# Kernel optimization log

Measured on AMD Instinct MI355X. Metric: run time of the kernel, lower is better.

Reference implementation:

```python
import jax, jax.numpy as jnp
import numpy as np

I_SIZE = 8      # interval_size
WS = 8          # window_size
SHIFT = 4       # window_size // 2
HG = 4          # grid-attn heads (num_heads // 2)
HS = 4          # swin/window heads (num_heads // 2)


def cln(x, g, b, eps=1e-5):
    # channel LayerNorm over axis 1 of NCHW
    mu = x.mean(axis=1, keepdims=True)
    var = ((x - mu) ** 2).mean(axis=1, keepdims=True)
    return (x - mu) / jnp.sqrt(var + eps) * g[None, :, None, None] + b[None, :, None, None]


def conv1x1(x, w, b):
    return jnp.einsum('bchw,oc->bohw', x, w) + b[None, :, None, None]


def grid_shuffle(x, I):
    B, C, H, W = x.shape
    H1, W1 = H // I, W // I
    x = x.reshape(B, C, H1, I, W1, I).transpose(0, 3, 5, 1, 2, 4)
    return x.reshape(B * I * I, C, H1, W1)


def grid_unshuffle(x, I):
    Bi, C, H1, W1 = x.shape
    B = Bi // (I * I)
    x = x.reshape(B, I, I, C, H1, W1).transpose(0, 3, 4, 1, 5, 2)
    return x.reshape(B, C, H1 * I, W1 * I)


def rel_pos_index(wh, ww):
    coords = np.stack(np.meshgrid(np.arange(wh), np.arange(ww), indexing='ij')).reshape(2, -1)
    rel = (coords[:, :, None] - coords[:, None, :]).transpose(1, 2, 0)
    rel[:, :, 0] += wh - 1
    rel[:, :, 1] += ww - 1
    rel[:, :, 0] *= 2 * ww - 1
    return rel.sum(-1)  # (N, N) int


def dyn_pos_bias(H1, W1, w1, b1, w2, b2, w3, b3):
    # dynamic position bias MLP: (2,) relative coords -> heads
    ch = np.arange(1 - H1, H1, dtype=np.float32)
    cw = np.arange(1 - W1, W1, dtype=np.float32)
    rel = np.stack(np.meshgrid(ch, cw, indexing='ij'), axis=-1).reshape(-1, 2)
    t = jnp.asarray(rel)
    t = jax.nn.relu(t @ w1.T + b1)
    t = jax.nn.relu(t @ w2.T + b2)
    t = t @ w3.T + b3  # ((2H1-1)*(2W1-1), heads)
    idx = rel_pos_index(H1, W1)
    return t[idx].transpose(2, 0, 1)[None]  # (1, heads, N, N)


def mha2d(q, k, v, bias, heads, pw, pb):
    B, C, H, W = q.shape
    hd, N = C // heads, H * W
    sp = lambda t: t.reshape(B, heads, hd, N).transpose(0, 1, 3, 2)
    qh, kh, vh = sp(q), sp(k), sp(v)
    attn = jax.nn.softmax(jnp.einsum('bhnd,bhmd->bhnm', qh * hd ** -0.5, kh) + bias, axis=-1)
    out = jnp.einsum('bhnm,bhmd->bhnd', attn, vh).transpose(0, 1, 3, 2).reshape(B, C, H, W)
    return conv1x1(out, pw, pb)


def swin_mask(H, W, ws, shift):
    img = np.zeros((H, W), np.float32)
    cnt = 0
    for hs in (slice(0, H - ws), slice(H - ws, H - shift), slice(H - shift, H)):
        for wsl in (slice(0, W - ws), slice(W - ws, W - shift), slice(W - shift, W)):
            img[hs, wsl] = cnt
            cnt += 1
    mw = img.reshape(H // ws, ws, W // ws, ws).transpose(0, 2, 1, 3).reshape(-1, ws * ws)
    m = mw[:, None, :] - mw[:, :, None]
    return jnp.asarray(np.where(m != 0, -100.0, 0.0).astype(np.float32))  # (nW, N, N)


def swin_attn(x, qkv_w, qkv_b, rpb, pw, pb, ws, shift, heads):
    B, C, H, W = x.shape
    hd, N = C // heads, ws * ws
    if shift > 0:
        x = jnp.roll(x, (-shift, -shift), axis=(2, 3))
    nh, nw = H // ws, W // ws
    nW = nh * nw
    xw = x.reshape(B, C, nh, ws, nw, ws).transpose(0, 2, 4, 3, 5, 1).reshape(B * nW, N, C)
    qkv = (xw @ qkv_w.T + qkv_b).reshape(B * nW, N, 3, heads, hd).transpose(2, 0, 3, 1, 4)
    q, k, v = qkv[0], qkv[1], qkv[2]
    attn = jnp.einsum('bhnd,bhmd->bhnm', q * hd ** -0.5, k)
    attn = attn + rpb[rel_pos_index(ws, ws)].transpose(2, 0, 1)[None]
    if shift > 0:
        mask = swin_mask(H, W, ws, shift)
        attn = (attn.reshape(B, nW, heads, N, N) + mask[None, :, None]).reshape(B * nW, heads, N, N)
    attn = jax.nn.softmax(attn, axis=-1)
    out = jnp.einsum('bhnm,bhmd->bhnd', attn, v).transpose(0, 2, 1, 3).reshape(B * nW, N, C)
    out = out @ pw.T + pb
    out = out.reshape(B, nh, nw, ws, ws, C).transpose(0, 5, 1, 3, 2, 4).reshape(B, C, H, W)
    if shift > 0:
        out = jnp.roll(out, (shift, shift), axis=(2, 3))
    return out


def setup_inputs() -> dict:
    ks = iter(jax.random.split(jax.random.key(0), 64))
    w = lambda *s: jax.random.normal(next(ks), s, jnp.float32) * 0.02
    d, dg, ds, hid = 128, 64, 32, 256
    return dict(
        x=jax.random.normal(next(ks), (4, d, 128, 128), jnp.float32),
        ln_g=jnp.ones(d), ln_b=jnp.zeros(d),
        ga_qkv_w=w(3 * dg, dg), ga_qkv_b=jnp.zeros(3 * dg),
        ga_gp_w=w(dg, dg), ga_gp_b=jnp.zeros(dg),
        pos_w1=w(16, 2), pos_b1=jnp.zeros(16),
        pos_w2=w(16, 16), pos_b2=jnp.zeros(16),
        pos_w3=w(HG, 16), pos_b3=jnp.zeros(HG),
        a1_pw=w(dg, dg), a1_pb=jnp.zeros(dg),
        a2_pw=w(dg, dg), a2_pb=jnp.zeros(dg),
        sw_qkv_w=w(3 * ds, ds), sw_qkv_b=jnp.zeros(3 * ds),
        sw_rpb=w((2 * WS - 1) ** 2, HS), sw_pw=w(ds, ds), sw_pb=jnp.zeros(ds),
        wn_qkv_w=w(3 * ds, ds), wn_qkv_b=jnp.zeros(3 * ds),
        wn_rpb=w((2 * WS - 1) ** 2, HS), wn_pw=w(ds, ds), wn_pb=jnp.zeros(ds),
        fc_w=w(d, d), fc_b=jnp.zeros(d),
        n2_g=jnp.ones(d), n2_b=jnp.zeros(d),
        m1_w=w(hid, d), m1_b=jnp.zeros(hid),
        m2_w=w(d, hid), m2_b=jnp.zeros(d),
    )


def reference(x, ln_g, ln_b, ga_qkv_w, ga_qkv_b, ga_gp_w, ga_gp_b,
              pos_w1, pos_b1, pos_w2, pos_b2, pos_w3, pos_b3,
              a1_pw, a1_pb, a2_pw, a2_pb,
              sw_qkv_w, sw_qkv_b, sw_rpb, sw_pw, sw_pb,
              wn_qkv_w, wn_qkv_b, wn_rpb, wn_pw, wn_pb,
              fc_w, fc_b, n2_g, n2_b, m1_w, m1_b, m2_w, m2_b):
    B, C, H, W = x.shape
    shortcut = x
    xg, xs, xw = jnp.split(x, [C // 2, C // 2 + C // 4], axis=1)

    # --- grid attention branch (C/2 channels) ---
    qkv = conv1x1(xg, ga_qkv_w, ga_qkv_b)
    x_grid = conv1x1(grid_shuffle(xg, I_SIZE), ga_gp_w, ga_gp_b)
    qkv = grid_shuffle(qkv, I_SIZE)
    H1, W1 = H // I_SIZE, W // I_SIZE
    pbias = dyn_pos_bias(H1, W1, pos_w1, pos_b1, pos_w2, pos_b2, pos_w3, pos_b3)
    q, k, v = jnp.split(qkv, 3, axis=1)
    t = mha2d(x_grid, k, v, pbias, HG, a1_pw, a1_pb)
    t = mha2d(q, x_grid, t, pbias, HG, a2_pw, a2_pb)
    xg_attn = grid_unshuffle(t, I_SIZE)

    # --- shifted / plain window attention branches (C/4 each) ---
    xs_attn = swin_attn(xs, sw_qkv_w, sw_qkv_b, sw_rpb, sw_pw, sw_pb, WS, SHIFT, HS)
    xw_attn = swin_attn(xw, wn_qkv_w, wn_qkv_b, wn_rpb, wn_pw, wn_pb, WS, 0, HS)

    x = jnp.concatenate([xw_attn, xs_attn, xg_attn], axis=1)
    x = cln(conv1x1(x, fc_w, fc_b), ln_g, ln_b)
    x = shortcut + x
    h = conv1x1(x, m1_w, m1_b)
    h = jax.nn.gelu(h, approximate=False)
    h = conv1x1(h, m2_w, m2_b)
    return x + cln(h, n2_g, n2_b) + shortcut
```

## Files before the change

### kernel.cpp

```cpp
#include <hip/hip_runtime.h>
#include <hip/hip_bf16.h>
#include <cstdint>


typedef __attribute__((ext_vector_type(8))) short bf8_t;
typedef __attribute__((ext_vector_type(4))) float f4_t;

__device__ __forceinline__ float bf2f(unsigned short u) {
  union { unsigned int i; float f; } x; x.i = ((unsigned int)u) << 16; return x.f;
}
__device__ __forceinline__ unsigned short f2bf(float f) {
  union { float f; unsigned int i; } x; x.f = f;
  unsigned int r = x.i + 0x7FFFu + ((x.i >> 16) & 1u);
  return (unsigned short)(r >> 16);
}
__device__ __forceinline__ unsigned int pk2(float a, float b) {
  unsigned int d;
  asm("v_cvt_pk_bf16_f32 %0, %1, %2" : "=v"(d) : "v"(a), "v"(b));
  return d;
}

#define MB (1048576L)

__global__ void pos_mlp_k(const float* __restrict__ w1, const float* __restrict__ b1,
                          const float* __restrict__ w2, const float* __restrict__ b2,
                          const float* __restrict__ w3, const float* __restrict__ b3,
                          float* __restrict__ table) {
  int j = blockIdx.x * 256 + threadIdx.x;
  if (j >= 961) return;
  float chv = (float)(j / 31) - 15.0f;
  float cwv = (float)(j % 31) - 15.0f;
  float t1[16], t2[16];
#pragma unroll
  for (int i = 0; i < 16; ++i) {
    float s = fmaf(w1[i * 2], chv, fmaf(w1[i * 2 + 1], cwv, b1[i]));
    t1[i] = fmaxf(s, 0.0f);
  }
#pragma unroll
  for (int i = 0; i < 16; ++i) {
    float s = b2[i];
#pragma unroll
    for (int k = 0; k < 16; ++k) s = fmaf(w2[i * 16 + k], t1[k], s);
    t2[i] = fmaxf(s, 0.0f);
  }
#pragma unroll
  for (int hh = 0; hh < 4; ++hh) {
    float s = b3[hh];
#pragma unroll
    for (int k = 0; k < 16; ++k) s = fmaf(w3[hh * 16 + k], t2[k], s);
    table[j * 4 + hh] = s;
  }
}

__global__ void pbT_gather_k(const float* __restrict__ table, float* __restrict__ pbT) {
  int t = blockIdx.x * 256 + threadIdx.x;
  int hh = t >> 16;
  int r = t & 65535;
  int m = r >> 8;
  int q = r & 255;
  int idx = ((q >> 4) - (m >> 4) + 15) * 31 + ((q & 15) - (m & 15) + 15);
  pbT[t] = table[idx * 4 + hh];
}

__global__ void rpbT_k(const float* __restrict__ rpb, float* __restrict__ rpbT) {
  int t = blockIdx.x * 256 + threadIdx.x;
  int h = t >> 12, r = t & 4095, m = r >> 6, n = r & 63;
  int idx = ((n >> 3) - (m >> 3) + 7) * 15 + ((n & 7) - (m & 7) + 7);
  rpbT[t] = rpb[idx * 4 + h];
}

__global__ void wq2_k(const float* __restrict__ sw_w, const float* __restrict__ sw_b,
                      const float* __restrict__ wn_w, const float* __restrict__ wn_b,
                      unsigned short* __restrict__ w2, float* __restrict__ b2) {
  const float QS = 0.35355339059327373f;
  int t = blockIdx.x * 256 + threadIdx.x;
  if (t < 12288) {
    int row = t >> 6, col = t & 63;
    float v = 0.0f;
    if (row < 96) { if (col < 32) v = sw_w[row * 32 + col]; }
    else          { if (col >= 32) v = wn_w[(row - 96) * 32 + col - 32]; }
    int rb = row % 96;
    if (rb < 32) v *= QS;
    w2[t] = f2bf(v);
  }
  if (t < 192) {
    float v = t < 96 ? sw_b[t] : wn_b[t - 96];
    if ((t % 96) < 32) v *= QS;
    b2[t] = v;
  }
}

__global__ void wcvt_k(const float* __restrict__ w0, const float* __restrict__ w1,
                       const float* __restrict__ w2, const float* __restrict__ w3,
                       const float* __restrict__ w4, const float* __restrict__ w5,
                       const float* __restrict__ w6,
                       const float* __restrict__ qkv_b, const float* __restrict__ gp_b,
                       unsigned short* __restrict__ dst, float* __restrict__ biasQG) {
  int t = blockIdx.x * 256 + threadIdx.x;
  if (t < 256) biasQG[t] = t < 192 ? qkv_b[t] : gp_b[t - 192] * 0.25f;
  if (t >= 106496) return;
  const float* src; int off; float sc = 1.0f;
  if (t < 12288)      { src = w0; off = 0; }
  else if (t < 16384) { src = w1; off = 12288; sc = 0.25f; }
  else if (t < 20480) { src = w2; off = 16384; }
  else if (t < 24576) { src = w3; off = 20480; }
  else if (t < 40960) { src = w4; off = 24576; }
  else if (t < 73728) { src = w5; off = 40960; }
  else                { src = w6; off = 73728; }
  dst[t] = f2bf(src[t - off] * sc);
}

__global__ __launch_bounds__(256) void tin_k(const float* __restrict__ x,
                                             unsigned short* __restrict__ xTb) {
  __shared__ float tile[64][132];
  const int b = blockIdx.z, px0 = blockIdx.x * 64, tid = threadIdx.x;
#pragma unroll
  for (int i = 0; i < 8; ++i) {
    int e = i * 256 + tid;
    int c = e >> 4, p4 = (e & 15) * 4;
    float4 v = *(const float4*)(x + (((size_t)(b * 128 + c)) << 14) + px0 + p4);
    tile[p4][c] = v.x; tile[p4 + 1][c] = v.y; tile[p4 + 2][c] = v.z; tile[p4 + 3][c] = v.w;
  }
  __syncthreads();
#pragma unroll
  for (int i = 0; i < 8; ++i) {
    int e = i * 256 + tid;
    int px = e >> 5, c4 = (e & 31) * 4;
    uint2 w = {pk2(tile[px][c4], tile[px][c4 + 1]), pk2(tile[px][c4 + 2], tile[px][c4 + 3])};
    *(uint2*)(xTb + ((size_t)(b * 16384 + px0 + px)) * 128 + c4) = w;
  }
}

template <int NF, int KC, int EPI, int OSHUF>
__global__ __launch_bounds__(256) void gemm_k(
    const unsigned short* __restrict__ A, int a_rs, int a_c0,
    const unsigned short* __restrict__ W, const float* __restrict__ bias,
    const float* __restrict__ g, const float* __restrict__ bb,
    const unsigned short* __restrict__ resf, const unsigned short* __restrict__ resb,
    void* __restrict__ out, int o_rs, int o_c0) {
  __shared__ __align__(16) char Asw[128 * 128];
  __shared__ __align__(16) char Bsw[NF * 16 * 128];
  const int tid = threadIdx.x;
  const int lane = tid & 63, wv = tid >> 6, wpx = wv * 32;
  const int lr = lane & 15, lg = lane >> 4;
  const int px0 = blockIdx.x * 128;
  const int co0 = blockIdx.y * (NF * 16);

  f4_t acc[2][NF];
#pragma unroll
  for (int mf = 0; mf < 2; ++mf)
#pragma unroll
    for (int nf = 0; nf < NF; ++nf) acc[mf][nf] = (f4_t){0.f, 0.f, 0.f, 0.f};

  for (int kc = 0; kc < KC; ++kc) {
    const int k0 = kc * 64;
    if (kc) __syncthreads();
#pragma unroll
    for (int i = 0; i < 4; ++i) {
      int e = i * 256 + tid;
      int row = e >> 3, q8 = e & 7;
      const unsigned short* src = A + (size_t)(px0 + row) * a_rs + a_c0 + k0 + q8 * 8;
      *(uint4*)(Asw + row * 128 + ((q8 ^ (row & 7)) << 4)) = *(const uint4*)src;
    }
#pragma unroll
    for (int i = 0; i < NF / 2; ++i) {
      int e = i * 256 + tid;
      int row = e >> 3, q8 = e & 7;
      const unsigned short* src = W + (size_t)(co0 + row) * (KC * 64) + k0 + q8 * 8;
      *(uint4*)(Bsw + row * 128 + ((q8 ^ (row & 7)) << 4)) = *(const uint4*)src;
    }
    __syncthreads();
#pragma unroll
    for (int ks = 0; ks < 2; ++ks) {
      const int xk = (((ks * 4) + lg) ^ (lane & 7)) << 4;
      bf8_t av[2], bv[NF];
#pragma unroll
      for (int mf = 0; mf < 2; ++mf)
        av[mf] = *(const bf8_t*)(Asw + (wpx + mf * 16 + lr) * 128 + xk);
#pragma unroll
      for (int nf = 0; nf < NF; ++nf)
        bv[nf] = *(const bf8_t*)(Bsw + (nf * 16 + lr) * 128 + xk);
#pragma unroll
      for (int mf = 0; mf < 2; ++mf)
#pragma unroll
        for (int nf = 0; nf < NF; ++nf)
          acc[mf][nf] = __builtin_amdgcn_mfma_f32_16x16x32_bf16(av[mf], bv[nf], acc[mf][nf], 0, 0, 0);
    }
  }

  float bco[NF];
#pragma unroll
  for (int nf = 0; nf < NF; ++nf) bco[nf] = bias[co0 + nf * 16 + lr];

  if constexpr (EPI >= 2) {
    float gv[NF], bbv[NF];
#pragma unroll
    for (int nf = 0; nf < NF; ++nf) { gv[nf] = g[nf * 16 + lr]; bbv[nf] = bb[nf * 16 + lr]; }
#pragma unroll
    for (int mf = 0; mf < 2; ++mf)
#pragma unroll
      for (int nf = 0; nf < NF; ++nf)
#pragma unroll
        for (int r = 0; r < 4; ++r) acc[mf][nf][r] += bco[nf];
#pragma unroll
    for (int mf = 0; mf < 2; ++mf) {
      float mus[4], rss[4];
#pragma unroll
      for (int r = 0; r < 4; ++r) {
        float s = 0.f, q = 0.f;
#pragma unroll
        for (int nf = 0; nf < NF; ++nf) {
          float v = acc[mf][nf][r];
          s += v; q += v * v;
        }
#pragma unroll
        for (int msk = 1; msk < 16; msk <<= 1) {
          s += __shfl_xor(s, msk);
          q += __shfl_xor(q, msk);
        }
        float mu = s * (1.0f / 128.0f);
        float var = q * (1.0f / 128.0f) - mu * mu;
        mus[r] = mu;
        rss[r] = rsqrtf(var + 1e-5f);
      }
      if constexpr (EPI == 2) {
#pragma unroll
        for (int r = 0; r < 4; ++r) {
          int px_e = px0 + wpx + mf * 16 + lg * 4 + r;
          const unsigned short* xr = resf + (size_t)px_e * 128 + lr;
          unsigned short* op = (unsigned short*)out + (size_t)px_e * o_rs + lr;
#pragma unroll
          for (int nf = 0; nf < NF; ++nf) {
            float v = (acc[mf][nf][r] - mus[r]) * rss[r] * gv[nf] + bbv[nf] + bf2f(xr[nf * 16]);
            op[nf * 16] = f2bf(v);
          }
        }
      } else {
        int pxb = px0 + wpx + mf * 16 + lg * 4;
        int b_ = pxb >> 14, p_ = pxb & 16383;
#pragma unroll
        for (int nf = 0; nf < NF; ++nf) {
          int ch = lr + nf * 16;
          float vr[4];
#pragma unroll
          for (int r = 0; r < 4; ++r) {
            float xv  = bf2f(resf[(size_t)(pxb + r) * 128 + ch]);
            float x2v = bf2f(resb[(size_t)(pxb + r) * 128 + ch]);
            vr[r] = (acc[mf][nf][r] - mus[r]) * rss[r] * gv[nf] + bbv[nf] + xv + x2v;
          }
          float4 v4 = {vr[0], vr[1], vr[2], vr[3]};
          *(float4*)((float*)out + (((size_t)(b_ * 128 + ch)) << 14) + p_) = v4;
        }
      }
    }
  } else {
#pragma unroll
    for (int mf = 0; mf < 2; ++mf) {
#pragma unroll
      for (int r = 0; r < 4; ++r) {
        int px_e = px0 + wpx + mf * 16 + lg * 4 + r;
        size_t orow;
        int cadj = co0;
        if constexpr (OSHUF == 0) {
          orow = (size_t)px_e;
        } else if constexpr (OSHUF == 1) {
          int b = px_e >> 14, p = px_e & 16383, hh = p >> 7, w_ = p & 127;
          orow = (size_t)(b * 64 + (hh & 7) * 8 + (w_ & 7)) * 256 + ((hh >> 3) * 16 + (w_ >> 3));
        } else if constexpr (OSHUF == 2) {
          int gbb = px_e >> 8, n = px_e & 255;
          int b = gbb >> 6, ih = (gbb >> 3) & 7, iw = gbb & 7;
          orow = (size_t)b * 16384 + ((n >> 4) * 8 + ih) * 128 + (n & 15) * 8 + iw;
        } else {
          int brx = (co0 >= 96);
          int b = px_e >> 14, p = px_e & 16383, hh = p >> 7, w_ = p & 127;
          int sh = brx ? 0 : 4;
          int h2 = (hh - sh) & 127, w2_ = (w_ - sh) & 127;
          orow = (size_t)brx * 65536 + (size_t)b * 16384 +
                 (size_t)(((h2 >> 3) * 16 + (w2_ >> 3)) * 64 + (h2 & 7) * 8 + (w2_ & 7));
          cadj = co0 - brx * 96;
        }
        unsigned short* op = (unsigned short*)out + orow * o_rs + o_c0 + cadj + lr;
#pragma unroll
        for (int nf = 0; nf < NF; ++nf) {
          float v = acc[mf][nf][r] + bco[nf];
          if constexpr (EPI == 1) v = 0.5f * v * (1.0f + erff(v * 0.7071067811865475f));
          op[nf * 16] = f2bf(v);
        }
      }
    }
  }
}

__global__ __launch_bounds__(256) void gattn_k(
    const unsigned short* __restrict__ Q, int q_rs, int q_c0,
    const unsigned short* __restrict__ K, int k_rs, int k_c0,
    const unsigned short* __restrict__ V, int v_rs, int v_c0,
    const float* __restrict__ pbT, unsigned short* __restrict__ outb, int o_rs, int o_c0) {
  __shared__ __align__(16) unsigned short K_lds[256 * 16];
  __shared__ __align__(16) unsigned short Vt[16 * 256];
  __shared__ __align__(16) unsigned short P_lds[4 * 64 * 32];
  const int gb = blockIdx.x, h = blockIdx.y, tid = threadIdx.x;
  const int lane = tid & 63, wv = tid >> 6;
  const int lr = lane & 15, lg = lane >> 4;
  const int q0 = wv * 64;

  {
    const unsigned short* kp = K + (size_t)(gb * 256 + tid) * k_rs + k_c0 + h * 16;
    *(uint4*)&K_lds[tid * 16]     = *(const uint4*)kp;
    *(uint4*)&K_lds[tid * 16 + 8] = *(const uint4*)(kp + 8);
    const unsigned short* vp = V + (size_t)(gb * 256 + tid) * v_rs + v_c0 + h * 16;
    uint4 va = *(const uint4*)vp;
    uint4 vb = *(const uint4*)(vp + 8);
    unsigned int w8[8] = {va.x, va.y, va.z, va.w, vb.x, vb.y, vb.z, vb.w};
    int chb = (tid >> 3);
    int wi = tid & 7;
#pragma unroll
    for (int w = 0; w < 8; ++w) {
      int d0 = 2 * w, d1 = 2 * w + 1;
      Vt[d0 * 256 + ((chb ^ (d0 & 7)) << 3) + wi] = (unsigned short)(w8[w] & 0xffff);
      Vt[d1 * 256 + ((chb ^ (d1 & 7)) << 3) + wi] = (unsigned short)(w8[w] >> 16);
    }
  }
  bf8_t bq[4];
  const bf8_t bz = {0, 0, 0, 0, 0, 0, 0, 0};
#pragma unroll
  for (int qt = 0; qt < 4; ++qt) {
    bq[qt] = bz;
    if (lg < 2)
      bq[qt] = *(const bf8_t*)(Q + (size_t)(gb * 256 + q0 + qt * 16 + lr) * q_rs + q_c0 + h * 16 + lg * 8);
  }
  __syncthreads();

  const f4_t z4 = {0.f, 0.f, 0.f, 0.f};
  f4_t oacc[4];
  float lrun[4];
#pragma unroll
  for (int qt = 0; qt < 4; ++qt) { oacc[qt] = z4; lrun[qt] = 0.0f; }

  unsigned short* Pw = &P_lds[wv * 64 * 32];

  for (int m0 = 0; m0 < 256; m0 += 32) {
    bf8_t ak0 = bz, ak1 = bz;
    if (lg < 2) {
      ak0 = *(const bf8_t*)&K_lds[(m0 + lr) * 16 + lg * 8];
      ak1 = *(const bf8_t*)&K_lds[(m0 + 16 + lr) * 16 + lg * 8];
    }
    bf8_t av = *(const bf8_t*)&Vt[lr * 256 + ((((m0 >> 3) + lg) ^ (lr & 7)) << 3)];

#pragma unroll
    for (int qt = 0; qt < 4; ++qt) {
      const float* bpm = pbT + ((size_t)(h * 256 + m0 + lg * 4) << 8) + q0 + qt * 16 + lr;
      f4_t c0v = {bpm[0], bpm[256], bpm[512], bpm[768]};
      f4_t c1v = {bpm[4096], bpm[4352], bpm[4608], bpm[4864]};
      f4_t st0 = __builtin_amdgcn_mfma_f32_16x16x32_bf16(ak0, bq[qt], c0v, 0, 0, 0);
      f4_t st1 = __builtin_amdgcn_mfma_f32_16x16x32_bf16(ak1, bq[qt], c1v, 0, 0, 0);
      float p0[4], p1[4], ls = 0.0f;
#pragma unroll
      for (int r = 0; r < 4; ++r) {
        p0[r] = __expf(st0[r]);
        p1[r] = __expf(st1[r]);
        ls += p0[r] + p1[r];
      }
      ls += __shfl_xor(ls, 16);
      ls += __shfl_xor(ls, 32);
      lrun[qt] += ls;
      int row = qt * 16 + lr;
      int rw3 = row & 3;
      uint2 w0 = {pk2(p0[0], p0[1]), pk2(p0[2], p0[3])};
      uint2 w1 = {pk2(p1[0], p1[1]), pk2(p1[2], p1[3])};
      *(uint2*)&Pw[row * 32 + ((((lg >> 1)) ^ rw3) << 3) + (lg & 1) * 4]     = w0;
      *(uint2*)&Pw[row * 32 + (((2 + (lg >> 1)) ^ rw3) << 3) + (lg & 1) * 4] = w1;
    }
#pragma unroll
    for (int qt = 0; qt < 4; ++qt) {
      int row = qt * 16 + lr;
      bf8_t bp = *(const bf8_t*)&Pw[row * 32 + ((lg ^ (row & 3)) << 3)];
      oacc[qt] = __builtin_amdgcn_mfma_f32_16x16x32_bf16(av, bp, oacc[qt], 0, 0, 0);
    }
  }

#pragma unroll
  for (int qt = 0; qt < 4; ++qt) {
    float inv = 1.0f / lrun[qt];
    uint2 o;
    o.x = pk2(oacc[qt][0] * inv, oacc[qt][1] * inv);
    o.y = pk2(oacc[qt][2] * inv, oacc[qt][3] * inv);
    unsigned short* op = outb + (size_t)(gb * 256 + q0 + qt * 16 + lr) * o_rs + o_c0 + h * 16 + lg * 4;
    *(uint2*)op = o;
  }
}

__global__ __launch_bounds__(256) void swat_k(
    const unsigned short* __restrict__ qkv2,
    const float* __restrict__ rpbT_sw, const float* __restrict__ rpbT_wn,
    const float* __restrict__ sw_pw, const float* __restrict__ sw_pb,
    const float* __restrict__ wn_pw, const float* __restrict__ wn_pb,
    unsigned short* __restrict__ yT) {
  __shared__ __align__(16) unsigned short Vt[4 * 8 * 64];
  __shared__ __align__(16) unsigned short Pt[4 * 64 * 64];
  __shared__ __align__(16) unsigned short aoT[4 * 64 * 32];
  const int tid = threadIdx.x, lane = tid & 63, wv = tid >> 6;
  const int lr = lane & 15, lg = lane >> 4;
  const int br = blockIdx.y;
  const int win = blockIdx.x * 4 + wv;
  const int b = win >> 8, wl = win & 255, wh = wl >> 4, ww = wl & 15;
  const float* rpbT = br ? rpbT_wn : rpbT_sw;
  const float* pw   = br ? wn_pw : sw_pw;
  const float* pb   = br ? wn_pb : sw_pb;
  const int shift = br ? 0 : 4;
  const int yc0 = br ? 0 : 32;
  const bool edge = (shift > 0) && (wh == 15 || ww == 15);

  const unsigned short* qw = qkv2 + (size_t)br * 65536 * 96 + (size_t)win * 64 * 96;
  const f4_t z4 = {0.f, 0.f, 0.f, 0.f};
  const bf8_t bz = {0, 0, 0, 0, 0, 0, 0, 0};
  unsigned short* Vw = &Vt[wv * 8 * 64];
  unsigned short* Pw = &Pt[wv * 64 * 64];
  unsigned short* aw_ = &aoT[wv * 64 * 32];

#pragma unroll 1
  for (int h = 0; h < 4; ++h) {
    {
      uint4 v = *(const uint4*)(qw + lane * 96 + 64 + h * 8);
      unsigned int w4[4] = {v.x, v.y, v.z, v.w};
      int chb = lane >> 3, wi = lane & 7;
#pragma unroll
      for (int j = 0; j < 4; ++j) {
        int d0 = 2 * j, d1 = 2 * j + 1;
        Vw[d0 * 64 + ((chb ^ (d0 & 7)) << 3) + wi] = (unsigned short)(w4[j] & 0xffff);
        Vw[d1 * 64 + ((chb ^ (d1 & 7)) << 3) + wi] = (unsigned short)(w4[j] >> 16);
      }
    }
    bf8_t bq[4];
#pragma unroll
    for (int nt = 0; nt < 4; ++nt) {
      bq[nt] = bz;
      if (lg == 0) bq[nt] = *(const bf8_t*)(qw + (nt * 16 + lr) * 96 + h * 8);
    }
    f4_t st[4][4];
#pragma unroll
    for (int mt = 0; mt < 4; ++mt) {
      bf8_t ak = bz;
      if (lg == 0) ak = *(const bf8_t*)(qw + (mt * 16 + lr) * 96 + 32 + h * 8);
#pragma unroll
      for (int nt = 0; nt < 4; ++nt) {
        const float* rp = rpbT + h * 4096 + (mt * 16 + lg * 4) * 64 + nt * 16 + lr;
        f4_t cb = {rp[0], rp[64], rp[128], rp[192]};
        st[mt][nt] = __builtin_amdgcn_mfma_f32_16x16x32_bf16(ak, bq[nt], cb, 0, 0, 0);
      }
    }
#pragma unroll
    for (int nt = 0; nt < 4; ++nt) {
      float sv[16];
#pragma unroll
      for (int mt = 0; mt < 4; ++mt)
#pragma unroll
        for (int r = 0; r < 4; ++r) sv[mt * 4 + r] = st[mt][nt][r];
      if (edge) {
        int n = nt * 16 + lr;
        int regn = ((wh < 15) ? 0 : (((n >> 3) < 4) ? 1 : 2)) * 3 +
                   ((ww < 15) ? 0 : (((n & 7) < 4) ? 1 : 2));
#pragma unroll
        for (int mt = 0; mt < 4; ++mt)
#pragma unroll
          for (int r = 0; r < 4; ++r) {
            int m = mt * 16 + lg * 4 + r;
            int regm = ((wh < 15) ? 0 : (((m >> 3) < 4) ? 1 : 2)) * 3 +
                       ((ww < 15) ? 0 : (((m & 7) < 4) ? 1 : 2));
            if (regm != regn) sv[mt * 4 + r] -= 100.0f;
          }
      }
      float l = 0.0f;
#pragma unroll
      for (int i = 0; i < 16; ++i) {
        sv[i] = __expf(sv[i]);
        l += sv[i];
      }
      l += __shfl_xor(l, 16);
      l += __shfl_xor(l, 32);
      float inv = 1.0f / l;
      int row = nt * 16 + lr, rw7 = lr & 7;
#pragma unroll
      for (int mt = 0; mt < 4; ++mt) {
        uint2 w = {pk2(sv[mt * 4] * inv, sv[mt * 4 + 1] * inv),
                   pk2(sv[mt * 4 + 2] * inv, sv[mt * 4 + 3] * inv)};
        *(uint2*)&Pw[row * 64 + (((2 * mt + (lg >> 1)) ^ rw7) << 3) + (lg & 1) * 4] = w;
      }
    }
    f4_t oa[4] = {z4, z4, z4, z4};
#pragma unroll
    for (int ks = 0; ks < 2; ++ks) {
      bf8_t av = bz;
      if (lr < 8) av = *(const bf8_t*)&Vw[lr * 64 + (((4 * ks + lg) ^ (lr & 7)) << 3)];
#pragma unroll
      for (int nt = 0; nt < 4; ++nt) {
        int row = nt * 16 + lr;
        bf8_t bp = *(const bf8_t*)&Pw[row * 64 + (((4 * ks + lg) ^ (lr & 7)) << 3)];
        oa[nt] = __builtin_amdgcn_mfma_f32_16x16x32_bf16(av, bp, oa[nt], 0, 0, 0);
      }
    }
    if (lg < 2) {
#pragma unroll
      for (int nt = 0; nt < 4; ++nt) {
        uint2 w = {pk2(oa[nt][0], oa[nt][1]), pk2(oa[nt][2], oa[nt][3])};
        int row = nt * 16 + lr;
        *(uint2*)&aw_[row * 32 + ((h ^ (lr & 3)) << 3) + lg * 4] = w;
      }
    }
  }

#pragma unroll
  for (int mt = 0; mt < 2; ++mt) {
    const float* wr = pw + (mt * 16 + lr) * 32 + lg * 8;
    float4 a0 = *(const float4*)wr, a1 = *(const float4*)(wr + 4);
    union { uint4 u; bf8_t v; } aw;
    aw.u.x = pk2(a0.x, a0.y); aw.u.y = pk2(a0.z, a0.w);
    aw.u.z = pk2(a1.x, a1.y); aw.u.w = pk2(a1.z, a1.w);
    float pb0 = pb[mt * 16 + lg * 4], pb1 = pb[mt * 16 + lg * 4 + 1];
    float pb2 = pb[mt * 16 + lg * 4 + 2], pb3 = pb[mt * 16 + lg * 4 + 3];
#pragma unroll
    for (int nt = 0; nt < 4; ++nt) {
      int row = nt * 16 + lr;
      bf8_t bo = *(const bf8_t*)&aw_[row * 32 + ((lg ^ (lr & 3)) << 3)];
      f4_t po = __builtin_amdgcn_mfma_f32_16x16x32_bf16(aw.v, bo, z4, 0, 0, 0);
      int n = nt * 16 + lr;
      int hdst = (wh * 8 + (n >> 3) + shift) & 127;
      int wdst = (ww * 8 + (n & 7) + shift) & 127;
      uint2 w = {pk2(po[0] + pb0, po[1] + pb1), pk2(po[2] + pb2, po[3] + pb3)};
      *(uint2*)(yT + ((size_t)(b * 16384 + hdst * 128 + wdst)) * 128 + yc0 + mt * 16 + lg * 4) = w;
    }
  }
}

extern "C" void kernel_launch(void* const* d_in, const int* in_sizes, int n_in,
                              void* d_out, int out_size, void* d_ws, size_t ws_size,
                              hipStream_t stream) {
  (void)in_sizes; (void)n_in; (void)out_size; (void)ws_size;
  const float* x        = (const float*)d_in[0];
  const float* ln_g     = (const float*)d_in[1];
  const float* ln_b     = (const float*)d_in[2];
  const float* ga_qkv_w = (const float*)d_in[3];
  const float* ga_qkv_b = (const float*)d_in[4];
  const float* ga_gp_w  = (const float*)d_in[5];
  const float* ga_gp_b  = (const float*)d_in[6];
  const float* pos_w1   = (const float*)d_in[7];
  const float* pos_b1   = (const float*)d_in[8];
  const float* pos_w2   = (const float*)d_in[9];
  const float* pos_b2   = (const float*)d_in[10];
  const float* pos_w3   = (const float*)d_in[11];
  const float* pos_b3   = (const float*)d_in[12];
  const float* a1_pw    = (const float*)d_in[13];
  const float* a1_pb    = (const float*)d_in[14];
  const float* a2_pw    = (const float*)d_in[15];
  const float* a2_pb    = (const float*)d_in[16];
  const float* sw_qkv_w = (const float*)d_in[17];
  const float* sw_qkv_b = (const float*)d_in[18];
  const float* sw_rpb   = (const float*)d_in[19];
  const float* sw_pw    = (const float*)d_in[20];
  const float* sw_pb    = (const float*)d_in[21];
  const float* wn_qkv_w = (const float*)d_in[22];
  const float* wn_qkv_b = (const float*)d_in[23];
  const float* wn_rpb   = (const float*)d_in[24];
  const float* wn_pw    = (const float*)d_in[25];
  const float* wn_pb    = (const float*)d_in[26];
  const float* fc_w     = (const float*)d_in[27];
  const float* fc_b     = (const float*)d_in[28];
  const float* n2_g     = (const float*)d_in[29];
  const float* n2_b     = (const float*)d_in[30];
  const float* m1_w     = (const float*)d_in[31];
  const float* m1_b     = (const float*)d_in[32];
  const float* m2_w     = (const float*)d_in[33];
  const float* m2_b     = (const float*)d_in[34];
  float* out = (float*)d_out;
  char* base = (char*)d_ws;

  unsigned short* xTb    = (unsigned short*)(base);
  unsigned short* qgT    = (unsigned short*)(base + 16 * MB);
  unsigned short* t1T    = (unsigned short*)(base + 48 * MB);
  unsigned short* t1pT   = (unsigned short*)(base + 56 * MB);
  unsigned short* yT     = (unsigned short*)(base + 64 * MB);
  unsigned short* x2T    = (unsigned short*)(base + 80 * MB);
  unsigned short* qkv2   = (unsigned short*)(base + 16 * MB);
  unsigned short* hT     = (unsigned short*)(base + 16 * MB);
  float*          pbT    = (float*)(base + 96 * MB);
  float*          ptab   = (float*)(base + 97 * MB);
  float*          rpbT_sw= (float*)(base + 97 * MB + 65536);
  float*          rpbT_wn= (float*)(base + 97 * MB + 131072);
  unsigned short* wq2bf  = (unsigned short*)(base + 97 * MB + 196608);
  float*          bias192= (float*)(base + 97 * MB + 229376);
  float*          biasQG = (float*)(base + 97 * MB + 230400);
  unsigned short* wbf    = (unsigned short*)(base + 97 * MB + 262144);

  pos_mlp_k<<<4, 256, 0, stream>>>(pos_w1, pos_b1, pos_w2, pos_b2, pos_w3, pos_b3, ptab);
  pbT_gather_k<<<1024, 256, 0, stream>>>(ptab, pbT);
  rpbT_k<<<64, 256, 0, stream>>>(sw_rpb, rpbT_sw);
  rpbT_k<<<64, 256, 0, stream>>>(wn_rpb, rpbT_wn);
  wq2_k<<<48, 256, 0, stream>>>(sw_qkv_w, sw_qkv_b, wn_qkv_w, wn_qkv_b, wq2bf, bias192);
  wcvt_k<<<416, 256, 0, stream>>>(ga_qkv_w, ga_gp_w, a1_pw, a2_pw, fc_w, m1_w, m2_w,
                                  ga_qkv_b, ga_gp_b, wbf, biasQG);

  tin_k<<<dim3(256, 1, 4), 256, 0, stream>>>(x, xTb);

  gemm_k<4, 1, 0, 1><<<dim3(512, 4, 1), 256, 0, stream>>>(
      xTb, 128, 0, wbf, biasQG, nullptr, nullptr, nullptr, nullptr, qgT, 256, 0);

  gattn_k<<<dim3(256, 4), 256, 0, stream>>>(
      qgT, 256, 192, qgT, 256, 64, qgT, 256, 128, pbT, t1T, 64, 0);
  gemm_k<4, 1, 0, 0><<<dim3(512, 1, 1), 256, 0, stream>>>(
      t1T, 64, 0, wbf + 16384, a1_pb, nullptr, nullptr, nullptr, nullptr, t1pT, 64, 0);

  gattn_k<<<dim3(256, 4), 256, 0, stream>>>(
      qgT, 256, 0, qgT, 256, 192, t1pT, 64, 0, pbT, t1T, 64, 0);
  gemm_k<4, 1, 0, 2><<<dim3(512, 1, 1), 256, 0, stream>>>(
      t1T, 64, 0, wbf + 20480, a2_pb, nullptr, nullptr, nullptr, nullptr, yT, 128, 64);

  gemm_k<6, 1, 0, 3><<<dim3(512, 2, 1), 256, 0, stream>>>(
      xTb, 128, 64, wq2bf, bias192, nullptr, nullptr, nullptr, nullptr, qkv2, 96, 0);
  swat_k<<<dim3(256, 2), 256, 0, stream>>>(
      qkv2, rpbT_sw, rpbT_wn, sw_pw, sw_pb, wn_pw, wn_pb, yT);

  gemm_k<8, 2, 2, 0><<<dim3(512, 1, 1), 256, 0, stream>>>(
      yT, 128, 0, wbf + 24576, fc_b, ln_g, ln_b, xTb, nullptr, x2T, 128, 0);

  gemm_k<8, 2, 1, 0><<<dim3(512, 2, 1), 256, 0, stream>>>(
      x2T, 128, 0, wbf + 40960, m1_b, nullptr, nullptr, nullptr, nullptr, hT, 256, 0);
  gemm_k<8, 4, 3, 0><<<dim3(512, 1, 1), 256, 0, stream>>>(
      hT, 256, 0, wbf + 73728, m2_b, n2_g, n2_b, xTb, x2T, out, 128, 0);
}
```

Measured before the change: 194.6 us.

## Merge setup kernels and store grid position bias as bf16 in query-major layout

Fuses five small weight/bias/position-table preparation kernels into a single setup launch, which removes several kernel launches. The grid-attention position bias is now stored as bf16 and transposed to query-major order, so each lane loads four contiguous bias values with one 8-byte load instead of eight strided fp32 scalar loads. This halves the bias bytes read per attention tile. The cost is that the bias added to the scores loses precision through bf16 rounding.

Result: slower. 206.5 us (+6.1%).

```diff
diff --git a/kernel.cpp b/kernel.cpp
--- a/kernel.cpp
+++ b/kernel.cpp
@@ -22,92 +22,93 @@
 
 #define MB (1048576L)
 
-__global__ void pos_mlp_k(const float* __restrict__ w1, const float* __restrict__ b1,
-                          const float* __restrict__ w2, const float* __restrict__ b2,
-                          const float* __restrict__ w3, const float* __restrict__ b3,
-                          float* __restrict__ table) {
-  int j = blockIdx.x * 256 + threadIdx.x;
-  if (j >= 961) return;
-  float chv = (float)(j / 31) - 15.0f;
-  float cwv = (float)(j % 31) - 15.0f;
-  float t1[16], t2[16];
-#pragma unroll
-  for (int i = 0; i < 16; ++i) {
-    float s = fmaf(w1[i * 2], chv, fmaf(w1[i * 2 + 1], cwv, b1[i]));
-    t1[i] = fmaxf(s, 0.0f);
-  }
-#pragma unroll
-  for (int i = 0; i < 16; ++i) {
-    float s = b2[i];
-#pragma unroll
-    for (int k = 0; k < 16; ++k) s = fmaf(w2[i * 16 + k], t1[k], s);
-    t2[i] = fmaxf(s, 0.0f);
-  }
-#pragma unroll
-  for (int hh = 0; hh < 4; ++hh) {
-    float s = b3[hh];
-#pragma unroll
-    for (int k = 0; k < 16; ++k) s = fmaf(w3[hh * 16 + k], t2[k], s);
-    table[j * 4 + hh] = s;
-  }
-}
-
-__global__ void pbT_gather_k(const float* __restrict__ table, float* __restrict__ pbT) {
-  int t = blockIdx.x * 256 + threadIdx.x;
-  int hh = t >> 16;
-  int r = t & 65535;
-  int m = r >> 8;
-  int q = r & 255;
-  int idx = ((q >> 4) - (m >> 4) + 15) * 31 + ((q & 15) - (m & 15) + 15);
-  pbT[t] = table[idx * 4 + hh];
-}
-
-__global__ void rpbT_k(const float* __restrict__ rpb, float* __restrict__ rpbT) {
-  int t = blockIdx.x * 256 + threadIdx.x;
-  int h = t >> 12, r = t & 4095, m = r >> 6, n = r & 63;
-  int idx = ((n >> 3) - (m >> 3) + 7) * 15 + ((n & 7) - (m & 7) + 7);
-  rpbT[t] = rpb[idx * 4 + h];
-}
-
-__global__ void wq2_k(const float* __restrict__ sw_w, const float* __restrict__ sw_b,
-                      const float* __restrict__ wn_w, const float* __restrict__ wn_b,
-                      unsigned short* __restrict__ w2, float* __restrict__ b2) {
+__global__ void setup_k(
+    const float* __restrict__ w0, const float* __restrict__ w1,
+    const float* __restrict__ w2, const float* __restrict__ w3,
+    const float* __restrict__ w4, const float* __restrict__ w5,
+    const float* __restrict__ w6,
+    const float* __restrict__ qkv_b, const float* __restrict__ gp_b,
+    const float* __restrict__ sw_w, const float* __restrict__ sw_b,
+    const float* __restrict__ wn_w, const float* __restrict__ wn_b,
+    const float* __restrict__ sw_rpb, const float* __restrict__ wn_rpb,
+    const float* __restrict__ pw1, const float* __restrict__ pb1,
+    const float* __restrict__ pw2, const float* __restrict__ pb2,
+    const float* __restrict__ pw3, const float* __restrict__ pb3,
+    unsigned short* __restrict__ wbf, float* __restrict__ biasQG,
+    unsigned short* __restrict__ wq2, float* __restrict__ b192,
+    float* __restrict__ rpbT_sw, float* __restrict__ rpbT_wn,
+    float* __restrict__ ptab) {
   const float QS = 0.35355339059327373f;
   int t = blockIdx.x * 256 + threadIdx.x;
-  if (t < 12288) {
-    int row = t >> 6, col = t & 63;
+  if (t < 106496) {
+    const float* src; int off; float sc = 1.0f;
+    if (t < 12288)      { src = w0; off = 0; }
+    else if (t < 16384) { src = w1; off = 12288; sc = 0.25f; }
+    else if (t < 20480) { src = w2; off = 16384; }
+    else if (t < 24576) { src = w3; off = 20480; }
+    else if (t < 40960) { src = w4; off = 24576; }
+    else if (t < 73728) { src = w5; off = 40960; }
+    else                { src = w6; off = 73728; }
+    wbf[t] = f2bf(src[t - off] * sc);
+  } else if (t < 106752) {
+    int i = t - 106496;
+    biasQG[i] = i < 192 ? qkv_b[i] : gp_b[i - 192] * 0.25f;
+  } else if (t < 119040) {
+    int i = t - 106752;
+    int row = i >> 6, col = i & 63;
     float v = 0.0f;
     if (row < 96) { if (col < 32) v = sw_w[row * 32 + col]; }
     else          { if (col >= 32) v = wn_w[(row - 96) * 32 + col - 32]; }
-    int rb = row % 96;
-    if (rb < 32) v *= QS;
-    w2[t] = f2bf(v);
-  }
-  if (t < 192) {
-    float v = t < 96 ? sw_b[t] : wn_b[t - 96];
-    if ((t % 96) < 32) v *= QS;
-    b2[t] = v;
-  }
-}
-
-__global__ void wcvt_k(const float* __restrict__ w0, const float* __restrict__ w1,
-                       const float* __restrict__ w2, const float* __restrict__ w3,
-                       const float* __restrict__ w4, const float* __restrict__ w5,
-                       const float* __restrict__ w6,
-                       const float* __restrict__ qkv_b, const float* __restrict__ gp_b,
-                       unsigned short* __restrict__ dst, float* __restrict__ biasQG) {
+    if ((row % 96) < 32) v *= QS;
+    wq2[i] = f2bf(v);
+  } else if (t < 119232) {
+    int i = t - 119040;
+    float v = i < 96 ? sw_b[i] : wn_b[i - 96];
+    if ((i % 96) < 32) v *= QS;
+    b192[i] = v;
+  } else if (t < 152000) {
+    int i = t - 119232;
+    const float* rpb = i < 16384 ? sw_rpb : wn_rpb;
+    float* dst = i < 16384 ? rpbT_sw : rpbT_wn;
+    int j = i & 16383;
+    int h = j >> 12, r = j & 4095, m = r >> 6, n = r & 63;
+    int idx = ((n >> 3) - (m >> 3) + 7) * 15 + ((n & 7) - (m & 7) + 7);
+    dst[j] = rpb[idx * 4 + h];
+  } else if (t < 152961) {
+    int j = t - 152000;
+    float chv = (float)(j / 31) - 15.0f;
+    float cwv = (float)(j % 31) - 15.0f;
+    float t1[16], t2[16];
+#pragma unroll
+    for (int i = 0; i < 16; ++i) {
+      float s = fmaf(pw1[i * 2], chv, fmaf(pw1[i * 2 + 1], cwv, pb1[i]));
+      t1[i] = fmaxf(s, 0.0f);
+    }
+#pragma unroll
+    for (int i = 0; i < 16; ++i) {
+      float s = pb2[i];
+#pragma unroll
+      for (int k = 0; k < 16; ++k) s = fmaf(pw2[i * 16 + k], t1[k], s);
+      t2[i] = fmaxf(s, 0.0f);
+    }
+#pragma unroll
+    for (int hh = 0; hh < 4; ++hh) {
+      float s = pb3[hh];
+#pragma unroll
+      for (int k = 0; k < 16; ++k) s = fmaf(pw3[hh * 16 + k], t2[k], s);
+      ptab[j * 4 + hh] = s;
+    }
+  }
+}
+
+__global__ void pbq_k(const float* __restrict__ table, unsigned short* __restrict__ pbTq) {
   int t = blockIdx.x * 256 + threadIdx.x;
-  if (t < 256) biasQG[t] = t < 192 ? qkv_b[t] : gp_b[t - 192] * 0.25f;
-  if (t >= 106496) return;
-  const float* src; int off; float sc = 1.0f;
-  if (t < 12288)      { src = w0; off = 0; }
-  else if (t < 16384) { src = w1; off = 12288; sc = 0.25f; }
-  else if (t < 20480) { src = w2; off = 16384; }
-  else if (t < 24576) { src = w3; off = 20480; }
-  else if (t < 40960) { src = w4; off = 24576; }
-  else if (t < 73728) { src = w5; off = 40960; }
-  else                { src = w6; off = 73728; }
-  dst[t] = f2bf(src[t - off] * sc);
+  int h = t >> 16;
+  int r = t & 65535;
+  int q = r >> 8;
+  int m = r & 255;
+  int idx = ((q >> 4) - (m >> 4) + 15) * 31 + ((q & 15) - (m & 15) + 15);
+  pbTq[t] = f2bf(table[idx * 4 + h]);
 }
 
 __global__ __launch_bounds__(256) void tin_k(const float* __restrict__ x,
@@ -295,7 +296,8 @@
     const unsigned short* __restrict__ Q, int q_rs, int q_c0,
     const unsigned short* __restrict__ K, int k_rs, int k_c0,
     const unsigned short* __restrict__ V, int v_rs, int v_c0,
-    const float* __restrict__ pbT, unsigned short* __restrict__ outb, int o_rs, int o_c0) {
+    const unsigned short* __restrict__ pbTq, unsigned short* __restrict__ outb,
+    int o_rs, int o_c0) {
   __shared__ __align__(16) unsigned short K_lds[256 * 16];
   __shared__ __align__(16) unsigned short Vt[16 * 256];
   __shared__ __align__(16) unsigned short P_lds[4 * 64 * 32];
@@ -349,9 +351,14 @@
 
 #pragma unroll
     for (int qt = 0; qt < 4; ++qt) {
-      const float* bpm = pbT + ((size_t)(h * 256 + m0 + lg * 4) << 8) + q0 + qt * 16 + lr;
-      f4_t c0v = {bpm[0], bpm[256], bpm[512], bpm[768]};
-      f4_t c1v = {bpm[4096], bpm[4352], bpm[4608], bpm[4864]};
+      const unsigned short* bq_ =
+          pbTq + (((size_t)(h * 256 + q0 + qt * 16 + lr)) << 8) + m0 + lg * 4;
+      uint2 u0 = *(const uint2*)bq_;
+      uint2 u1 = *(const uint2*)(bq_ + 16);
+      f4_t c0v = {bf2f((unsigned short)u0.x), bf2f((unsigned short)(u0.x >> 16)),
+                  bf2f((unsigned short)u0.y), bf2f((unsigned short)(u0.y >> 16))};
+      f4_t c1v = {bf2f((unsigned short)u1.x), bf2f((unsigned short)(u1.x >> 16)),
+                  bf2f((unsigned short)u1.y), bf2f((unsigned short)(u1.y >> 16))};
       f4_t st0 = __builtin_amdgcn_mfma_f32_16x16x32_bf16(ak0, bq[qt], c0v, 0, 0, 0);
       f4_t st1 = __builtin_amdgcn_mfma_f32_16x16x32_bf16(ak1, bq[qt], c1v, 0, 0, 0);
       float p0[4], p1[4], ls = 0.0f;
@@ -582,7 +589,7 @@
   unsigned short* x2T    = (unsigned short*)(base + 80 * MB);
   unsigned short* qkv2   = (unsigned short*)(base + 16 * MB);
   unsigned short* hT     = (unsigned short*)(base + 16 * MB);
-  float*          pbT    = (float*)(base + 96 * MB);
+  unsigned short* pbTq   = (unsigned short*)(base + 96 * MB);
   float*          ptab   = (float*)(base + 97 * MB);
   float*          rpbT_sw= (float*)(base + 97 * MB + 65536);
   float*          rpbT_wn= (float*)(base + 97 * MB + 131072);
@@ -591,13 +598,14 @@
   float*          biasQG = (float*)(base + 97 * MB + 230400);
   unsigned short* wbf    = (unsigned short*)(base + 97 * MB + 262144);
 
-  pos_mlp_k<<<4, 256, 0, stream>>>(pos_w1, pos_b1, pos_w2, pos_b2, pos_w3, pos_b3, ptab);
-  pbT_gather_k<<<1024, 256, 0, stream>>>(ptab, pbT);
-  rpbT_k<<<64, 256, 0, stream>>>(sw_rpb, rpbT_sw);
-  rpbT_k<<<64, 256, 0, stream>>>(wn_rpb, rpbT_wn);
-  wq2_k<<<48, 256, 0, stream>>>(sw_qkv_w, sw_qkv_b, wn_qkv_w, wn_qkv_b, wq2bf, bias192);
-  wcvt_k<<<416, 256, 0, stream>>>(ga_qkv_w, ga_gp_w, a1_pw, a2_pw, fc_w, m1_w, m2_w,
-                                  ga_qkv_b, ga_gp_b, wbf, biasQG);
+  setup_k<<<598, 256, 0, stream>>>(
+      ga_qkv_w, ga_gp_w, a1_pw, a2_pw, fc_w, m1_w, m2_w,
+      ga_qkv_b, ga_gp_b,
+      sw_qkv_w, sw_qkv_b, wn_qkv_w, wn_qkv_b,
+      sw_rpb, wn_rpb,
+      pos_w1, pos_b1, pos_w2, pos_b2, pos_w3, pos_b3,
+      wbf, biasQG, wq2bf, bias192, rpbT_sw, rpbT_wn, ptab);
+  pbq_k<<<1024, 256, 0, stream>>>(ptab, pbTq);
 
   tin_k<<<dim3(256, 1, 4), 256, 0, stream>>>(x, xTb);
 
@@ -605,12 +613,12 @@
       xTb, 128, 0, wbf, biasQG, nullptr, nullptr, nullptr, nullptr, qgT, 256, 0);
 
   gattn_k<<<dim3(256, 4), 256, 0, stream>>>(
-      qgT, 256, 192, qgT, 256, 64, qgT, 256, 128, pbT, t1T, 64, 0);
+      qgT, 256, 192, qgT, 256, 64, qgT, 256, 128, pbTq, t1T, 64, 0);
   gemm_k<4, 1, 0, 0><<<dim3(512, 1, 1), 256, 0, stream>>>(
       t1T, 64, 0, wbf + 16384, a1_pb, nullptr, nullptr, nullptr, nullptr, t1pT, 64, 0);
 
   gattn_k<<<dim3(256, 4), 256, 0, stream>>>(
-      qgT, 256, 0, qgT, 256, 192, t1pT, 64, 0, pbT, t1T, 64, 0);
+      qgT, 256, 0, qgT, 256, 192, t1pT, 64, 0, pbTq, t1T, 64, 0);
   gemm_k<4, 1, 0, 2><<<dim3(512, 1, 1), 256, 0, stream>>>(
       t1T, 64, 0, wbf + 20480, a2_pb, nullptr, nullptr, nullptr, nullptr, yT, 128, 64);
 
```
